# Kernel tuning notes

Measured on AMD Instinct MI355X. Metric: run time of the kernel, lower is better.

## Reference

```python
import jax, jax.numpy as jnp
import numpy as np

B, N_ATOM, COORD = 32, 48, 3
N_ELEM = 4
GRID_SIZE = 128
SIGMA = 0.05      # gaussian broadening of distf
W_SCALE = 1.0     # weightf: exp(-W_SCALE * distance)
INV_SQRT2PI = 1.0 / np.sqrt(2.0 * np.pi)


def _pairs(n):
    # static ordered index pairs i != j (built with numpy -> jit-safe constants)
    ii, jj = np.meshgrid(np.arange(n), np.arange(n), indexing='ij')
    m = ii != jj
    return jnp.asarray(ii[m]), jnp.asarray(jj[m])


def setup_inputs() -> dict:
    key = jax.random.key(0)
    k1, k2 = jax.random.split(key)
    r = jax.random.normal(k1, (B, N_ATOM, COORD), dtype=jnp.float32) * 2.0
    z = jax.random.randint(k2, (N_ATOM,), 0, N_ELEM)  # species index in [0, N_ELEM)
    grid = jnp.linspace(0.0, 2.0, GRID_SIZE, dtype=jnp.float32)
    return {"r": r, "z": z, "grid": grid}


def reference(r, z, grid):
    b, n, c = r.shape
    g = grid.shape[0]
    e = N_ELEM
    dx = grid[1] - grid[0]
    pi, pj = _pairs(n)                              # (P,)

    diff = r[:, pi] - r[:, pj]                      # (b,P,3)
    d = jnp.sqrt(jnp.sum(diff * diff, axis=-1))     # (b,P) pair distances
    gf = 1.0 / d                                    # geomf: inverse distance
    wf = jnp.exp(-W_SCALE * d)                      # weightf: exponential decay
    # distf: normalized gaussian centered at gf, scaled by grid spacing dx
    t = (grid[None, None, :] - gf[..., None]) / SIGMA
    gv = jnp.exp(-0.5 * t * t) * (dx * INV_SQRT2PI / SIGMA)   # (b,P,G)

    contrib = wf[..., None] * gv                    # (b,P,G)
    seg = z[pi] * e + z[pj]                         # (P,) element-pair bucket
    mbtr = jax.ops.segment_sum(contrib.transpose(1, 0, 2), seg, num_segments=e * e)
    mbtr = mbtr.reshape(e, e, b, g).transpose(2, 0, 1, 3)      # (b,E,E,G)

    # analytic divergence wrt the two atoms' coordinates (order=2, coord=3)
    u = diff / d[..., None]                         # dd/dr_i, (b,P,3)
    dd = jnp.stack([u, -u], axis=2)                 # (b,P,2,3): dd/dr_{i}, dd/dr_{j}
    gf_div = -(gf * gf)[..., None, None] * dd       # d(1/d)/dr
    wf_div = -(W_SCALE * wf)[..., None, None] * dd  # d exp(-s d)/dr
    grid_div = gv * (grid[None, None, :] - gf[..., None]) / (SIGMA * SIGMA)  # dgv/dgf

    # (b,P,G,2,3): gv*wf_div + grid_div*gf_div*wf
    div = (gv[:, :, :, None, None] * wf_div[:, :, None, :, :]
           + grid_div[:, :, :, None, None] * (gf_div * wf[..., None, None])[:, :, None, :, :])

    atom_idx = jnp.stack([pi, pj], axis=1)          # (P,2)
    seg_div = (seg[:, None] * n + atom_idx).reshape(-1)        # (2P,) bucket*n + atom
    p2 = div.transpose(1, 3, 0, 2, 4).reshape(-1, b, g, c)     # (2P,b,G,3)
    mbtr_div = jax.ops.segment_sum(p2, seg_div, num_segments=e * e * n)
    mbtr_div = mbtr_div.reshape(e, e, n, b, g, c).transpose(3, 0, 1, 4, 2, 5)  # (b,E,E,G,N,3)
    return mbtr, mbtr_div
```

## Files before the change

### kernel.cpp

```cpp
#include <hip/hip_runtime.h>

#define NB     32
#define NATOM  48
#define NGRID  128
#define KT     8
#define NTHR   384

#define MBTR_ELEMS (NB*16*NGRID)
#define DIV_PER_B  (16*NGRID*NATOM*3)
#define PANE       (NGRID*NATOM*3)
#define MSTRIDE    49

__global__ __launch_bounds__(NTHR)
void mbtr_fused(const float* __restrict__ r, const int* __restrict__ z,
                const float* __restrict__ grid, float* __restrict__ out)
{
    const int kt = blockIdx.x, b = blockIdx.y, t = threadIdx.x;
    const int k0 = kt * KT;

    __shared__ float4 pos_s[NATOM + 1];
    __shared__ int    zl[NATOM];
    __shared__ int    soff_s[5];
    __shared__ float  znpos[NATOM * 3];
    __shared__ float  Mrec[KT * 4 * MSTRIDE];

    if (t < 64) {
        const bool isatom = (t < NATOM);
        int myz = 999;
        float rx = 0.f, ry = 0.f, rz = 0.f;
        if (isatom) {
            myz = z[t];
            zl[t] = myz;
            const float* rp = r + ((size_t)b * NATOM + t) * 3;
            rx = rp[0]; ry = rp[1]; rz = rp[2];
            znpos[t * 3 + 0] = rx; znpos[t * 3 + 1] = ry; znpos[t * 3 + 2] = rz;
        }
        const unsigned long long m0 = __ballot(myz == 0);
        const unsigned long long m1 = __ballot(myz == 1);
        const unsigned long long m2 = __ballot(myz == 2);
        const unsigned long long m3 = __ballot(myz == 3);
        const int c0 = __popcll(m0), c1 = __popcll(m1), c2 = __popcll(m2);
        if (isatom) {
            const unsigned long long mm = (myz == 0) ? m0 : (myz == 1) ? m1
                                        : (myz == 2) ? m2 : m3;
            const int base = (myz == 0) ? 0 : (myz == 1) ? c0
                           : (myz == 2) ? c0 + c1 : c0 + c1 + c2;
            const int rank = __popcll(mm & ((1ull << t) - 1ull));
            pos_s[base + rank] = make_float4(rx, ry, rz, (float)t);
        }
        if (t == 0) {
            soff_s[0] = 0; soff_s[1] = c0; soff_s[2] = c0 + c1;
            soff_s[3] = c0 + c1 + c2; soff_s[4] = NATOM;
            pos_s[NATOM] = make_float4(0.f, 0.f, 0.f, -1.f);
        }
    }
    __syncthreads();

    const int n  = t % NATOM;
    const int kk = t / NATOM;
    const float dx   = grid[1] - grid[0];
    const float coef = dx * 7.9788456080286535f;
    const float mlc  = -__log2f(coef);
    const float isc  = 16.986436005760382f;
    const float tBc  = 23.548200452219559f;
    const float l2e  = 1.4426950408889634f;
    const float gk   = grid[k0 + kk] * isc;
    const float nf   = (float)n;

    float A[4][3] = {{0.f}};
    float M[4]    = {0.f};
    const float rnx = znpos[n * 3 + 0];
    const float rny = znpos[n * 3 + 1];
    const float rnz = znpos[n * 3 + 2];
    const int   zn  = zl[n];
    int so[5];
    #pragma unroll
    for (int e = 0; e < 5; ++e) so[e] = soff_s[e];

    #pragma unroll
    for (int e = 0; e < 4; ++e) {
        #pragma unroll 4
        for (int i = so[e]; i < so[e + 1]; ++i) {
            const float4 rm = pos_s[i];
            const float ddx = rnx - rm.x, ddy = rny - rm.y, ddz = rnz - rm.z;
            float d2 = ddx*ddx + ddy*ddy + ddz*ddz;
            const bool self = (rm.w == nf);
            d2 = self ? 1.0f : d2;
            const float gf  = __builtin_amdgcn_rsqf(d2);
            const float c1  = gf * isc;
            const float d   = d2 * gf;
            float base = fmaf(d, l2e, mlc);
            base = self ? 1e30f : base;
            const float bq  = (gf * gf) * tBc;
            const float tt  = gk - c1;
            const float ex  = exp2f(-fmaf(tt, tt, base));
            M[e] += ex;
            const float p   = ex * fmaf(tt, bq, 1.0f);
            A[e][0] = fmaf(-p, gf * ddx, A[e][0]);
            A[e][1] = fmaf(-p, gf * ddy, A[e][1]);
            A[e][2] = fmaf(-p, gf * ddz, A[e][2]);
        }
    }

    {
        float* mr = Mrec + kk * (4 * MSTRIDE) + n;
        #pragma unroll
        for (int e = 0; e < 4; ++e) mr[e * MSTRIDE] = M[e];
    }

    float* basep = out + MBTR_ELEMS + (size_t)b * DIV_PER_B
                 + (size_t)(k0 + kk) * 144 + n * 3;
    #pragma unroll
    for (int e1 = 0; e1 < 4; ++e1) {
        const bool s1 = (zn == e1);
        #pragma unroll
        for (int e2 = 0; e2 < 4; ++e2) {
            const bool s2 = (zn == e2);
            float3 v;
            v.x = (s1 ? A[e2][0] : 0.f) + (s2 ? A[e1][0] : 0.f);
            v.y = (s1 ? A[e2][1] : 0.f) + (s2 ? A[e1][1] : 0.f);
            v.z = (s1 ? A[e2][2] : 0.f) + (s2 ? A[e1][2] : 0.f);
            *(float3*)(basep + (e1 * 4 + e2) * PANE) = v;
        }
    }

    __syncthreads();

    if (t < 128) {
        const int mpane = t >> 3, mkk = t & 7;
        const int me1 = mpane >> 2, me2 = mpane & 3;
        const float* tr2 = Mrec + mkk * (4 * MSTRIDE) + me2 * MSTRIDE;
        float s = 0.f;
        #pragma unroll
        for (int nn = 0; nn < NATOM; ++nn)
            s += (zl[nn] == me1) ? tr2[nn] : 0.f;
        out[(size_t)b * 2048 + mpane * NGRID + k0 + mkk] = s;
    }
}

extern "C" void kernel_launch(void* const* d_in, const int* in_sizes, int n_in,
                              void* d_out, int out_size, void* d_ws, size_t ws_size,
                              hipStream_t stream)
{
    const float* r    = (const float*)d_in[0];
    const int*   z    = (const int*)  d_in[1];
    const float* grid = (const float*)d_in[2];
    float* out = (float*)d_out;
    (void)d_ws; (void)ws_size;

    mbtr_fused<<<dim3(NGRID / KT, NB), NTHR, 0, stream>>>(r, z, grid, out);
}
```

Measured before the change: 80.70 us.

## Split pair loop across two thread halves with shared-memory partial reduction

Doubles the block size to 768 threads and has each half process alternate partner atoms, then combines the partial A/M accumulators through a new shared-memory buffer. The mbtr reduction moves to the second half so it can run while the first half writes the divergence output. The goal is more latency hiding per block and a shorter serial loop per thread, at the cost of extra shared memory, an additional barrier, and lower per-CU block occupancy.

```diff
diff --git a/kernel.cpp b/kernel.cpp
--- a/kernel.cpp
+++ b/kernel.cpp
@@ -4,12 +4,13 @@
 #define NATOM  48
 #define NGRID  128
 #define KT     8
-#define NTHR   384
+#define NTHR   768
 
 #define MBTR_ELEMS (NB*16*NGRID)
 #define DIV_PER_B  (16*NGRID*NATOM*3)
 #define PANE       (NGRID*NATOM*3)
 #define MSTRIDE    49
+#define PSTRIDE    17
 
 __global__ __launch_bounds__(NTHR)
 void mbtr_fused(const float* __restrict__ r, const int* __restrict__ z,
@@ -23,6 +24,7 @@
     __shared__ int    soff_s[5];
     __shared__ float  znpos[NATOM * 3];
     __shared__ float  Mrec[KT * 4 * MSTRIDE];
+    __shared__ float  Part[384 * PSTRIDE];
 
     if (t < 64) {
         const bool isatom = (t < NATOM);
@@ -56,8 +58,10 @@
     }
     __syncthreads();
 
-    const int n  = t % NATOM;
-    const int kk = t / NATOM;
+    const int h  = (t < 384) ? 0 : 1;
+    const int tt = t - 384 * h;
+    const int n  = tt % NATOM;
+    const int kk = tt / NATOM;
     const float dx   = grid[1] - grid[0];
     const float coef = dx * 7.9788456080286535f;
     const float mlc  = -__log2f(coef);
@@ -79,8 +83,8 @@
 
     #pragma unroll
     for (int e = 0; e < 4; ++e) {
-        #pragma unroll 4
-        for (int i = so[e]; i < so[e + 1]; ++i) {
+        #pragma unroll 2
+        for (int i = so[e] + h; i < so[e + 1]; i += 2) {
             const float4 rm = pos_s[i];
             const float ddx = rnx - rm.x, ddy = rny - rm.y, ddz = rnz - rm.z;
             float d2 = ddx*ddx + ddy*ddy + ddz*ddz;
@@ -92,42 +96,60 @@
             float base = fmaf(d, l2e, mlc);
             base = self ? 1e30f : base;
             const float bq  = (gf * gf) * tBc;
-            const float tt  = gk - c1;
-            const float ex  = exp2f(-fmaf(tt, tt, base));
+            const float tt2 = gk - c1;
+            const float ex  = exp2f(-fmaf(tt2, tt2, base));
             M[e] += ex;
-            const float p   = ex * fmaf(tt, bq, 1.0f);
+            const float p   = ex * fmaf(tt2, bq, 1.0f);
             A[e][0] = fmaf(-p, gf * ddx, A[e][0]);
             A[e][1] = fmaf(-p, gf * ddy, A[e][1]);
             A[e][2] = fmaf(-p, gf * ddz, A[e][2]);
         }
     }
 
-    {
+    if (h == 1) {
+        float* pp = Part + tt * PSTRIDE;
+        #pragma unroll
+        for (int e = 0; e < 4; ++e) {
+            pp[e * 3 + 0] = A[e][0];
+            pp[e * 3 + 1] = A[e][1];
+            pp[e * 3 + 2] = A[e][2];
+            pp[12 + e]    = M[e];
+        }
+    }
+    __syncthreads();
+    if (h == 0) {
+        const float* pp = Part + tt * PSTRIDE;
+        #pragma unroll
+        for (int e = 0; e < 4; ++e) {
+            A[e][0] += pp[e * 3 + 0];
+            A[e][1] += pp[e * 3 + 1];
+            A[e][2] += pp[e * 3 + 2];
+            M[e]    += pp[12 + e];
+        }
         float* mr = Mrec + kk * (4 * MSTRIDE) + n;
         #pragma unroll
         for (int e = 0; e < 4; ++e) mr[e * MSTRIDE] = M[e];
     }
-
-    float* basep = out + MBTR_ELEMS + (size_t)b * DIV_PER_B
-                 + (size_t)(k0 + kk) * 144 + n * 3;
-    #pragma unroll
-    for (int e1 = 0; e1 < 4; ++e1) {
-        const bool s1 = (zn == e1);
-        #pragma unroll
-        for (int e2 = 0; e2 < 4; ++e2) {
-            const bool s2 = (zn == e2);
-            float3 v;
-            v.x = (s1 ? A[e2][0] : 0.f) + (s2 ? A[e1][0] : 0.f);
-            v.y = (s1 ? A[e2][1] : 0.f) + (s2 ? A[e1][1] : 0.f);
-            v.z = (s1 ? A[e2][2] : 0.f) + (s2 ? A[e1][2] : 0.f);
-            *(float3*)(basep + (e1 * 4 + e2) * PANE) = v;
-        }
-    }
-
     __syncthreads();
 
-    if (t < 128) {
-        const int mpane = t >> 3, mkk = t & 7;
+    if (h == 0) {
+        float* basep = out + MBTR_ELEMS + (size_t)b * DIV_PER_B
+                     + (size_t)(k0 + kk) * 144 + n * 3;
+        #pragma unroll
+        for (int e1 = 0; e1 < 4; ++e1) {
+            const bool s1 = (zn == e1);
+            #pragma unroll
+            for (int e2 = 0; e2 < 4; ++e2) {
+                const bool s2 = (zn == e2);
+                float3 v;
+                v.x = (s1 ? A[e2][0] : 0.f) + (s2 ? A[e1][0] : 0.f);
+                v.y = (s1 ? A[e2][1] : 0.f) + (s2 ? A[e1][1] : 0.f);
+                v.z = (s1 ? A[e2][2] : 0.f) + (s2 ? A[e1][2] : 0.f);
+                *(float3*)(basep + (e1 * 4 + e2) * PANE) = v;
+            }
+        }
+    } else if (tt < 128) {
+        const int mpane = tt >> 3, mkk = tt & 7;
         const int me1 = mpane >> 2, me2 = mpane & 3;
         const float* tr2 = Mrec + mkk * (4 * MSTRIDE) + me2 * MSTRIDE;
         float s = 0.f;
```

Result: no change. 80.25 us (-0.6%).
